# Performance work log

Hardware: AMD Instinct MI355X
Metric: run time of the kernel (lower is better)

## Reference

```python
import jax, jax.numpy as jnp
import numpy as np

HID = 256
VOCAB = 1000
REPEAT = 32
ALPHA = 1.0
LBR = 0.2
THRESH = 0.8 * ALPHA * (1.0 - LBR)  # 0.64


def _lstm_layer(x, Wih, Whh, bih, bhh):
    # x: [B,S,D]; returns hidden states [S,B,H] (torch gate order i,f,g,o)
    B = x.shape[0]
    H = Whh.shape[1]
    xg = jnp.einsum('bsd,gd->sbg', x, Wih) + (bih + bhh)  # [S,B,4H]
    def step(carry, gx):
        h, c = carry
        g = gx + h @ Whh.T
        i, f, gg, o = jnp.split(g, 4, axis=-1)
        c = jax.nn.sigmoid(f) * c + jax.nn.sigmoid(i) * jnp.tanh(gg)
        h = jax.nn.sigmoid(o) * jnp.tanh(c)
        return (h, c), h
    init = (jnp.zeros((B, H), x.dtype), jnp.zeros((B, H), x.dtype))
    _, hs = jax.lax.scan(step, init, xg)
    return hs


def _encode(x, Wih0, Whh0, bih0, bhh0, Wih1, Whh1, bih1, bhh1):
    # 2-layer LSTM (dropout inactive at inference), then sum over time -> [B,H]
    hs = _lstm_layer(x, Wih0, Whh0, bih0, bhh0)                      # [S,B,H]
    hs = _lstm_layer(jnp.transpose(hs, (1, 0, 2)), Wih1, Whh1, bih1, bhh1)
    return hs.sum(0)


def setup_inputs():
    key = jax.random.key(0)
    ks = jax.random.split(key, 20)
    B, S, D, H, P = 64, 128, 64, HID, 1024
    s = jnp.float32(0.05)
    return {
        'x1': jax.random.normal(ks[0], (B, S, D), jnp.float32),
        'x2': jax.random.normal(ks[1], (B, S, D), jnp.float32),
        'Wih0': s * jax.random.normal(ks[2], (4 * H, D), jnp.float32),
        'Whh0': s * jax.random.normal(ks[3], (4 * H, H), jnp.float32),
        'bih0': s * jax.random.normal(ks[4], (4 * H,), jnp.float32),
        'bhh0': s * jax.random.normal(ks[5], (4 * H,), jnp.float32),
        'Wih1': s * jax.random.normal(ks[6], (4 * H, H), jnp.float32),
        'Whh1': s * jax.random.normal(ks[7], (4 * H, H), jnp.float32),
        'bih1': s * jax.random.normal(ks[8], (4 * H,), jnp.float32),
        'bhh1': s * jax.random.normal(ks[9], (4 * H,), jnp.float32),
        'fc1_w': s * jax.random.normal(ks[10], (P, 2 * H), jnp.float32),
        'fc1_b': s * jax.random.normal(ks[11], (P,), jnp.float32),
        'fc2_w': s * jax.random.normal(ks[12], (P, P), jnp.float32),
        'fc2_b': s * jax.random.normal(ks[13], (P,), jnp.float32),
        'fc3_w': s * jax.random.normal(ks[14], (VOCAB * REPEAT, P), jnp.float32),
        'fc3_b': s * jax.random.normal(ks[15], (VOCAB * REPEAT,), jnp.float32),
        'bn_g': jnp.ones((P,), jnp.float32),
        'bn_b': jnp.zeros((P,), jnp.float32),
    }


def reference(x1, x2, Wih0, Whh0, bih0, bhh0, Wih1, Whh1, bih1, bhh1,
              fc1_w, fc1_b, fc2_w, fc2_b, fc3_w, fc3_b, bn_g, bn_b):
    out1 = _encode(x1, Wih0, Whh0, bih0, bhh0, Wih1, Whh1, bih1, bhh1)
    out2 = _encode(x2, Wih0, Whh0, bih0, bhh0, Wih1, Whh1, bih1, bhh1)
    h = jnp.concatenate([out1, out2], axis=1)                # [B,2H]
    h = jax.nn.gelu(h @ fc1_w.T + fc1_b, approximate=False)  # exact gelu (torch)
    h = h + jax.nn.relu(h @ fc2_w.T + fc2_b)
    # BatchNorm1d with batch statistics (training-mode normalization)
    mu = h.mean(0)
    var = h.var(0)
    h = (h - mu) / jnp.sqrt(var + 1e-5) * bn_g + bn_b
    scores = jax.nn.relu(h @ fc3_w.T + fc3_b)
    scores = scores.reshape(-1, VOCAB, REPEAT)               # [B,V,R]
    # vectorized replacement of the per-row .item() selection loop:
    # number of atoms selected per row at threshold 0.8*alpha*(1-lbr)
    num_select = jnp.maximum(1, (scores > THRESH).sum(axis=(1, 2)))
    return scores, num_select
```

## Files before the change

### kernel.cpp

```cpp
#include <hip/hip_runtime.h>
#include <cmath>


typedef _Float16 f16;
typedef _Float16 f16x8 __attribute__((ext_vector_type(8)));
typedef _Float16 f16x4 __attribute__((ext_vector_type(4)));
typedef float f32x4 __attribute__((ext_vector_type(4)));

#define MFMA(a,b,c) __builtin_amdgcn_mfma_f32_16x16x32_f16((a),(b),(c),0,0,0)
#define LSTR 280

__device__ __forceinline__ float frcp(float x) { return __builtin_amdgcn_rcpf(x); }
__device__ __forceinline__ float sigf(float x)  { return frcp(1.f + __expf(-x)); }
__device__ __forceinline__ float tanhf_(float x){ return 1.f - 2.f*frcp(__expf(2.f*x) + 1.f); }

__global__ void k_convert(const float* __restrict__ x1, const float* __restrict__ x2,
                          const float* __restrict__ Wih0, const float* __restrict__ Whh0,
                          const float* __restrict__ bih0, const float* __restrict__ bhh0,
                          const float* __restrict__ Wih1, const float* __restrict__ Whh1,
                          const float* __restrict__ bih1, const float* __restrict__ bhh1,
                          f16* __restrict__ x16, f16* __restrict__ w16, float* __restrict__ bsum,
                          int* __restrict__ flg)
{
    int i = blockIdx.x * 256 + threadIdx.x;
    if (i < 524288) { x16[i] = (f16)x1[i]; x16[524288 + i] = (f16)x2[i]; }
    if (i < 65536)  w16[i] = (f16)Wih0[i];
    if (i < 262144) {
        w16[65536  + i] = (f16)Whh0[i];
        w16[327680 + i] = (f16)Wih1[i];
        w16[589824 + i] = (f16)Whh1[i];
    }
    if (i < 1024) { bsum[i] = bih0[i] + bhh0[i]; bsum[1024 + i] = bih1[i] + bhh1[i]; }
    if (i < 64) flg[i] = 0;
}

template<int K>
__global__ __launch_bounds__(512)
void k_proj(const f16* __restrict__ A, const f16* __restrict__ Bw,
            const float* __restrict__ bias, f16* __restrict__ out)
{
    const int w = threadIdx.x >> 6, lane = threadIdx.x & 63;
    const int quad = lane >> 4, l16 = lane & 15;
    const long m0 = (long)blockIdx.x * 128 + w * 16;
    f32x4 acc[2][4] = {};
    #pragma unroll
    for (int kc = 0; kc < K/32; ++kc) {
        const int ko = kc*32 + quad*8;
        f16x8 a = *(const f16x8*)(A + (m0 + l16)*K + ko);
        #pragma unroll
        for (int tg = 0; tg < 2; ++tg) {
            const int ti = blockIdx.y*2 + tg;
            #pragma unroll
            for (int g = 0; g < 4; ++g) {
                f16x8 b = *(const f16x8*)(Bw + (long)(g*256 + ti*16 + l16)*K + ko);
                acc[tg][g] = MFMA(a, b, acc[tg][g]);
            }
        }
    }
    #pragma unroll
    for (int tg = 0; tg < 2; ++tg) {
        const int ti = blockIdx.y*2 + tg;
        float bi[4];
        #pragma unroll
        for (int g = 0; g < 4; ++g) bi[g] = bias[g*256 + ti*16 + l16];
        #pragma unroll
        for (int r = 0; r < 4; ++r) {
            long mm = m0 + quad*4 + r;
            f16x4 pv;
            #pragma unroll
            for (int g = 0; g < 4; ++g) pv[g] = (f16)(acc[tg][g][r] + bi[g]);
            *(f16x4*)(out + mm*1024 + ti*64 + l16*4) = pv;
        }
    }
}

__global__ __launch_bounds__(512, 2)
void k_mega(const f16* __restrict__ w16, const f16* __restrict__ xg0,
            f16* __restrict__ xg1, f16* __restrict__ h0s,
            const float* __restrict__ bsum1, float* __restrict__ out_enc,
            int* __restrict__ flags)
{
    __shared__ f16 wl[256*LSTR];
    __shared__ f16 hb[2*16*LSTR];
    const int tid = threadIdx.x;
    const int w = tid >> 6, lane = tid & 63;
    const int quad = lane >> 4, l16 = lane & 15;
    const int role = blockIdx.x >> 3, g = blockIdx.x & 7;

    const f16* W = (role == 0) ? w16 + 65536
                 : (role == 1) ? w16 + 327680
                               : w16 + 589824;

    f16x8 bres[6][8];
    #pragma unroll
    for (int s6 = 0; s6 < 6; ++s6) {
        const int tile = (s6 >> 1)*16 + 2*w + (s6 & 1);
        #pragma unroll
        for (int kc = 0; kc < 8; ++kc)
            bres[s6][kc] = *(const f16x8*)(W + (tile*16 + l16)*256 + kc*32 + quad*8);
    }
    {
        const int r = tid >> 1, hh = tid & 1;
        const f16* src = W + (768 + r)*256 + hh*128;
        f16* dst = wl + r*LSTR + hh*128;
        #pragma unroll
        for (int j = 0; j < 16; ++j)
            *(f16x8*)(dst + j*8) = *(const f16x8*)(src + j*8);
    }

    if (role == 1) {
        float bi[2][4];
        #pragma unroll
        for (int q = 0; q < 2; ++q)
            #pragma unroll
            for (int g4 = 0; g4 < 4; ++g4) bi[q][g4] = bsum1[g4*256 + (2*w+q)*16 + l16];
        __syncthreads();
        #pragma unroll 1
        for (int s = 0; s < 128; ++s) {
            if (tid == 0) {
                while (__hip_atomic_load(&flags[g], __ATOMIC_ACQUIRE,
                                         __HIP_MEMORY_SCOPE_AGENT) < s + 1)
                    __builtin_amdgcn_s_sleep(2);
            }
            __syncthreads();
            const f16* hrow = h0s + ((long)s*128 + g*16 + l16)*256 + quad*8;
            f16x8 av[8];
            #pragma unroll
            for (int kc = 0; kc < 8; ++kc) av[kc] = *(const f16x8*)(hrow + kc*32);
            #pragma unroll
            for (int q = 0; q < 2; ++q) {
                const int ti = 2*w + q;
                f32x4 ai = {}, af = {}, ag = {}, ao = {};
                #pragma unroll
                for (int kc = 0; kc < 8; ++kc) {
                    f16x8 bo = *(const f16x8*)(wl + (ti*16 + l16)*LSTR + kc*32 + quad*8);
                    ai = MFMA(av[kc], bres[q][kc],   ai);
                    af = MFMA(av[kc], bres[2+q][kc], af);
                    ag = MFMA(av[kc], bres[4+q][kc], ag);
                    ao = MFMA(av[kc], bo,            ao);
                }
                #pragma unroll
                for (int r = 0; r < 4; ++r) {
                    f16x4 pv;
                    pv[0] = (f16)(ai[r] + bi[q][0]);
                    pv[1] = (f16)(af[r] + bi[q][1]);
                    pv[2] = (f16)(ag[r] + bi[q][2]);
                    pv[3] = (f16)(ao[r] + bi[q][3]);
                    *(f16x4*)(xg1 + ((long)(g*16 + quad*4 + r)*128 + s)*1024
                                  + ti*64 + l16*4) = pv;
                }
            }
            __syncthreads();
            if (tid == 0)
                __hip_atomic_store(&flags[8+g], s + 1, __ATOMIC_RELEASE,
                                   __HIP_MEMORY_SCOPE_AGENT);
        }
        return;
    }

    for (int i = tid; i < 2*16*LSTR; i += 512) hb[i] = (f16)0.f;

    const f16* xg = (role == 0) ? xg0 : xg1;
    const f16* xp[4];
    #pragma unroll
    for (int r = 0; r < 4; ++r)
        xp[r] = xg + (long)(g*16 + quad*4 + r)*131072 + (2*w)*64 + l16*4;

    float c[8]    = {0,0,0,0,0,0,0,0};
    float oacc[8] = {0,0,0,0,0,0,0,0};
    __syncthreads();

    #pragma unroll 1
    for (int s = 0; s < 128; ++s) {
        const int rb = s & 1, wb = rb ^ 1;
        if (role == 2) {
            if (tid == 0) {
                while (__hip_atomic_load(&flags[8+g], __ATOMIC_ACQUIRE,
                                         __HIP_MEMORY_SCOPE_AGENT) < s + 1)
                    __builtin_amdgcn_s_sleep(2);
            }
            __syncthreads();
        }
        if (role == 0 && s > 0) {
            const int cc = tid >> 5, kk = (tid & 31) * 8;
            f16x8 hv = *(const f16x8*)(hb + (rb*16 + cc)*LSTR + kk);
            *(f16x8*)(h0s + ((long)(s-1)*128 + g*16 + cc)*256 + kk) = hv;
        }
        f16x4 xv[2][4];
        #pragma unroll
        for (int r = 0; r < 4; ++r) {
            xv[0][r] = *(const f16x4*)(xp[r]);
            xv[1][r] = *(const f16x4*)(xp[r] + 64);
        }
        #pragma unroll
        for (int q = 0; q < 2; ++q) {
            const int ti = 2*w + q;
            f32x4 ai = {}, af = {}, ag = {}, ao = {};
            #pragma unroll
            for (int kc = 0; kc < 8; ++kc) {
                f16x8 a  = *(const f16x8*)(hb + (rb*16 + l16)*LSTR + kc*32 + quad*8);
                f16x8 bo = *(const f16x8*)(wl + (ti*16 + l16)*LSTR + kc*32 + quad*8);
                ai = MFMA(a, bres[q][kc],   ai);
                af = MFMA(a, bres[2+q][kc], af);
                ag = MFMA(a, bres[4+q][kc], ag);
                ao = MFMA(a, bo,            ao);
            }
            #pragma unroll
            for (int r = 0; r < 4; ++r) {
                float gi = sigf(ai[r] + (float)xv[q][r][0]);
                float gf = sigf(af[r] + (float)xv[q][r][1]);
                float gg = tanhf_(ag[r] + (float)xv[q][r][2]);
                float go = sigf(ao[r] + (float)xv[q][r][3]);
                const int ci = q*4 + r;
                float cn = gf*c[ci] + gi*gg;
                c[ci] = cn;
                float hn = go * tanhf_(cn);
                if (role == 2) oacc[ci] += hn;
                hb[(wb*16 + quad*4 + r)*LSTR + ti*16 + l16] = (f16)hn;
            }
        }
        #pragma unroll
        for (int r = 0; r < 4; ++r) xp[r] += 1024;
        __syncthreads();
        if (role == 0 && tid == 0)
            __hip_atomic_store(&flags[g], s, __ATOMIC_RELEASE,
                               __HIP_MEMORY_SCOPE_AGENT);
    }
    if (role == 0) {
        const int cc = tid >> 5, kk = (tid & 31) * 8;
        f16x8 hv = *(const f16x8*)(hb + (0*16 + cc)*LSTR + kk);
        *(f16x8*)(h0s + ((long)127*128 + g*16 + cc)*256 + kk) = hv;
        __syncthreads();
        if (tid == 0)
            __hip_atomic_store(&flags[g], 128, __ATOMIC_RELEASE,
                               __HIP_MEMORY_SCOPE_AGENT);
    }
    if (role == 2) {
        #pragma unroll
        for (int q = 0; q < 2; ++q)
            #pragma unroll
            for (int r = 0; r < 4; ++r)
                out_enc[(long)(g*16 + quad*4 + r)*256 + (2*w+q)*16 + l16] = oacc[q*4 + r];
    }
}

template<int K, int MODE>
__global__ __launch_bounds__(256)
void k_fc(const float* __restrict__ A, const float* __restrict__ W,
          const float* __restrict__ bias, const float* __restrict__ res,
          float* __restrict__ out, const int Nst)
{
    __shared__ float ws[32*64];
    __shared__ float as[64*64];
    const int tid = threadIdx.x;
    const int n0 = blockIdx.x * 32;
    const int m2 = tid & 31, ndg = tid >> 5;
    float acc[2][4] = {};
    for (int kc = 0; kc < K/64; ++kc) {
        __syncthreads();
        {
            const int col = tid >> 3, k8 = (tid & 7)*8;
            const float* src = W + (long)(n0 + col)*K + kc*64 + k8;
            *(float4*)(ws + col*64 + k8)     = *(const float4*)(src);
            *(float4*)(ws + col*64 + k8 + 4) = *(const float4*)(src + 4);
        }
        {
            const int m = tid >> 2, j4 = (tid & 3)*16;
            #pragma unroll
            for (int i4 = 0; i4 < 4; ++i4) {
                const int kk = kc*64 + j4 + i4*4;
                const float* srcA;
                if (MODE == 0) srcA = (kk < 256) ? (A + (long)m*256 + kk)
                                                 : (A + 16384 + (long)m*256 + kk - 256);
                else           srcA = A + (long)m*K + kk;
                float4 v = *(const float4*)srcA;
                as[(j4 + i4*4 + 0)*64 + m] = v.x;
                as[(j4 + i4*4 + 1)*64 + m] = v.y;
                as[(j4 + i4*4 + 2)*64 + m] = v.z;
                as[(j4 + i4*4 + 3)*64 + m] = v.w;
            }
        }
        __syncthreads();
        #pragma unroll 4
        for (int k4 = 0; k4 < 64; k4 += 4) {
            float a0[4], a1[4];
            #pragma unroll
            for (int i = 0; i < 4; ++i) {
                a0[i] = as[(k4+i)*64 + m2];
                a1[i] = as[(k4+i)*64 + m2 + 32];
            }
            #pragma unroll
            for (int j = 0; j < 4; ++j) {
                const float4 wv = *(const float4*)(ws + (ndg*4 + j)*64 + k4);
                acc[0][j] += a0[0]*wv.x + a0[1]*wv.y + a0[2]*wv.z + a0[3]*wv.w;
                acc[1][j] += a1[0]*wv.x + a1[1]*wv.y + a1[2]*wv.z + a1[3]*wv.w;
            }
        }
    }
    #pragma unroll
    for (int i = 0; i < 2; ++i) {
        const int m = m2 + i*32;
        #pragma unroll
        for (int j = 0; j < 4; ++j) {
            const int nn = n0 + ndg*4 + j;
            float v = acc[i][j] + bias[nn];
            if (MODE == 0)      v = 0.5f * v * (1.0f + erff(v * 0.7071067811865475f));
            else if (MODE == 1) v = res[(long)m*1024 + nn] + fmaxf(v, 0.f);
            else                v = fmaxf(v, 0.f);
            out[(long)m*Nst + nn] = v;
        }
    }
}

__global__ void k_bn(const float* __restrict__ h2, const float* __restrict__ g,
                     const float* __restrict__ b, float* __restrict__ h3)
{
    const int col = blockIdx.x*256 + threadIdx.x;
    float s = 0.f, ss = 0.f;
    for (int m = 0; m < 64; ++m) { float v = h2[m*1024 + col]; s += v; ss += v*v; }
    const float mu  = s * (1.f/64.f);
    const float var = ss * (1.f/64.f) - mu*mu;
    const float rs  = rsqrtf(var + 1e-5f);
    const float gg = g[col], bb = b[col];
    for (int m = 0; m < 64; ++m) {
        float v = h2[m*1024 + col];
        h3[m*1024 + col] = (v - mu)*rs*gg + bb;
    }
}

__global__ void k_count(const float* __restrict__ scores, float* __restrict__ outc)
{
    const int row = blockIdx.x, tid = threadIdx.x;
    const float* p = scores + (long)row*32000;
    int cnt = 0;
    for (int i = tid; i < 32000; i += 256)
        cnt += ((double)p[i] > 0.6400000000000001) ? 1 : 0;
    __shared__ int red[256];
    red[tid] = cnt; __syncthreads();
    for (int off = 128; off > 0; off >>= 1) {
        if (tid < off) red[tid] += red[tid + off];
        __syncthreads();
    }
    if (tid == 0) outc[row] = (float)(red[0] < 1 ? 1 : red[0]);
}

extern "C" void kernel_launch(void* const* d_in, const int* in_sizes, int n_in,
                              void* d_out, int out_size, void* d_ws, size_t ws_size,
                              hipStream_t stream)
{
    const float* x1    = (const float*)d_in[0];
    const float* x2    = (const float*)d_in[1];
    const float* Wih0  = (const float*)d_in[2];
    const float* Whh0  = (const float*)d_in[3];
    const float* bih0  = (const float*)d_in[4];
    const float* bhh0  = (const float*)d_in[5];
    const float* Wih1  = (const float*)d_in[6];
    const float* Whh1  = (const float*)d_in[7];
    const float* bih1  = (const float*)d_in[8];
    const float* bhh1  = (const float*)d_in[9];
    const float* fc1_w = (const float*)d_in[10];
    const float* fc1_b = (const float*)d_in[11];
    const float* fc2_w = (const float*)d_in[12];
    const float* fc2_b = (const float*)d_in[13];
    const float* fc3_w = (const float*)d_in[14];
    const float* fc3_b = (const float*)d_in[15];
    const float* bn_g  = (const float*)d_in[16];
    const float* bn_b  = (const float*)d_in[17];
    float* out = (float*)d_out;

    char* ws = (char*)d_ws;
    f16*   x16   = (f16*)(ws);
    f16*   w16   = (f16*)(ws + 2097152);
    float* bsum  = (float*)(ws + 3801088);
    int*   flags = (int*)(ws + 3809280);
    float* enc   = (float*)(ws + 3809536);
    f16*   h0s   = (f16*)(ws + 3940608);
    f16*   xg0   = (f16*)(ws + 12329216);
    f16*   xg1   = (f16*)(ws + 45883648);
    float* h1    = (float*)(ws + 12329216);
    float* h2    = (float*)(ws + 12591360);
    float* h3    = (float*)(ws + 12853504);

    k_convert<<<2048, 256, 0, stream>>>(x1,x2,Wih0,Whh0,bih0,bhh0,Wih1,Whh1,bih1,bhh1,
                                        x16, w16, bsum, flags);
    k_proj<64><<<dim3(128,8), 512, 0, stream>>>(x16, w16, bsum, xg0);
    k_mega<<<24, 512, 0, stream>>>(w16, xg0, xg1, h0s, bsum + 1024, enc, flags);
    k_fc<512,0><<<32, 256, 0, stream>>>(enc, fc1_w, fc1_b, nullptr, h1, 1024);
    k_fc<1024,1><<<32, 256, 0, stream>>>(h1, fc2_w, fc2_b, h1, h2, 1024);
    k_bn<<<4, 256, 0, stream>>>(h2, bn_g, bn_b, h3);
    k_fc<1024,2><<<1000, 256, 0, stream>>>(h3, fc3_w, fc3_b, nullptr, out, 32000);
    k_count<<<64, 256, 0, stream>>>(out, out + 2048000);
}
```

Before: 1.036 ms.

## Batch LSTM cross-block flag handshakes every two steps and fuse BatchNorm into fc2

The producer/consumer flag synchronisation between the layer-0 recurrence, the layer-1 input projection and the layer-1 recurrence blocks now happens every two timesteps instead of every step. Spin-waits use relaxed polling followed by a single acquire load. Separately, the BatchNorm statistics and normalisation are fused into the fc2 epilogue through a shared-memory transpose, which removes the k_bn launch and one intermediate buffer. This lowers per-step synchronisation latency in the serial critical path, at the cost of coarser pipelining granularity between stages.

```diff
diff --git a/kernel.cpp b/kernel.cpp
--- a/kernel.cpp
+++ b/kernel.cpp
@@ -13,6 +13,12 @@
 __device__ __forceinline__ float frcp(float x) { return __builtin_amdgcn_rcpf(x); }
 __device__ __forceinline__ float sigf(float x)  { return frcp(1.f + __expf(-x)); }
 __device__ __forceinline__ float tanhf_(float x){ return 1.f - 2.f*frcp(__expf(2.f*x) + 1.f); }
+
+__device__ __forceinline__ void wait_flag(int* f, int target) {
+    while (__hip_atomic_load(f, __ATOMIC_RELAXED, __HIP_MEMORY_SCOPE_AGENT) < target)
+        __builtin_amdgcn_s_sleep(1);
+    (void)__hip_atomic_load(f, __ATOMIC_ACQUIRE, __HIP_MEMORY_SCOPE_AGENT);
+}
 
 __global__ void k_convert(const float* __restrict__ x1, const float* __restrict__ x2,
                           const float* __restrict__ Wih0, const float* __restrict__ Whh0,
@@ -117,12 +123,10 @@
         __syncthreads();
         #pragma unroll 1
         for (int s = 0; s < 128; ++s) {
-            if (tid == 0) {
-                while (__hip_atomic_load(&flags[g], __ATOMIC_ACQUIRE,
-                                         __HIP_MEMORY_SCOPE_AGENT) < s + 1)
-                    __builtin_amdgcn_s_sleep(2);
-            }
-            __syncthreads();
+            if ((s & 1) == 0) {
+                if (tid == 0) wait_flag(&flags[g], s + 2);
+                __syncthreads();
+            }
             const f16* hrow = h0s + ((long)s*128 + g*16 + l16)*256 + quad*8;
             f16x8 av[8];
             #pragma unroll
@@ -150,10 +154,12 @@
                                   + ti*64 + l16*4) = pv;
                 }
             }
-            __syncthreads();
-            if (tid == 0)
-                __hip_atomic_store(&flags[8+g], s + 1, __ATOMIC_RELEASE,
-                                   __HIP_MEMORY_SCOPE_AGENT);
+            if (s & 1) {
+                __syncthreads();
+                if (tid == 0)
+                    __hip_atomic_store(&flags[8+g], s + 1, __ATOMIC_RELEASE,
+                                       __HIP_MEMORY_SCOPE_AGENT);
+            }
         }
         return;
     }
@@ -173,12 +179,8 @@
     #pragma unroll 1
     for (int s = 0; s < 128; ++s) {
         const int rb = s & 1, wb = rb ^ 1;
-        if (role == 2) {
-            if (tid == 0) {
-                while (__hip_atomic_load(&flags[8+g], __ATOMIC_ACQUIRE,
-                                         __HIP_MEMORY_SCOPE_AGENT) < s + 1)
-                    __builtin_amdgcn_s_sleep(2);
-            }
+        if (role == 2 && (s & 1) == 0) {
+            if (tid == 0) wait_flag(&flags[8+g], s + 2);
             __syncthreads();
         }
         if (role == 0 && s > 0) {
@@ -222,7 +224,7 @@
         #pragma unroll
         for (int r = 0; r < 4; ++r) xp[r] += 1024;
         __syncthreads();
-        if (role == 0 && tid == 0)
+        if (role == 0 && (s & 1) == 0 && s > 0 && tid == 0)
             __hip_atomic_store(&flags[g], s, __ATOMIC_RELEASE,
                                __HIP_MEMORY_SCOPE_AGENT);
     }
@@ -248,10 +250,12 @@
 __global__ __launch_bounds__(256)
 void k_fc(const float* __restrict__ A, const float* __restrict__ W,
           const float* __restrict__ bias, const float* __restrict__ res,
+          const float* __restrict__ bng, const float* __restrict__ bnb,
           float* __restrict__ out, const int Nst)
 {
     __shared__ float ws[32*64];
     __shared__ float as[64*64];
+    __shared__ float mus[32], rss[32];
     const int tid = threadIdx.x;
     const int n0 = blockIdx.x * 32;
     const int m2 = tid & 31, ndg = tid >> 5;
@@ -297,6 +301,43 @@
             }
         }
     }
+    if (MODE == 1) {
+        float vv[2][4];
+        #pragma unroll
+        for (int i = 0; i < 2; ++i)
+            #pragma unroll
+            for (int j = 0; j < 4; ++j) {
+                const int m = m2 + i*32, nn = n0 + ndg*4 + j;
+                vv[i][j] = res[(long)m*1024 + nn] + fmaxf(acc[i][j] + bias[nn], 0.f);
+            }
+        __syncthreads();
+        #pragma unroll
+        for (int i = 0; i < 2; ++i)
+            #pragma unroll
+            for (int j = 0; j < 4; ++j)
+                as[(m2 + i*32)*33 + ndg*4 + j] = vv[i][j];
+        __syncthreads();
+        if (tid < 32) {
+            float s = 0.f, ss = 0.f;
+            #pragma unroll 4
+            for (int m = 0; m < 64; ++m) {
+                float x = as[m*33 + tid];
+                s += x; ss += x*x;
+            }
+            const float mu = s * (1.f/64.f);
+            mus[tid] = mu;
+            rss[tid] = rsqrtf(ss * (1.f/64.f) - mu*mu + 1e-5f);
+        }
+        __syncthreads();
+        #pragma unroll
+        for (int i = 0; i < 2; ++i)
+            #pragma unroll
+            for (int j = 0; j < 4; ++j) {
+                const int m = m2 + i*32, cl = ndg*4 + j, nn = n0 + cl;
+                out[(long)m*Nst + nn] = (vv[i][j] - mus[cl]) * rss[cl] * bng[nn] + bnb[nn];
+            }
+        return;
+    }
     #pragma unroll
     for (int i = 0; i < 2; ++i) {
         const int m = m2 + i*32;
@@ -304,27 +345,10 @@
         for (int j = 0; j < 4; ++j) {
             const int nn = n0 + ndg*4 + j;
             float v = acc[i][j] + bias[nn];
-            if (MODE == 0)      v = 0.5f * v * (1.0f + erff(v * 0.7071067811865475f));
-            else if (MODE == 1) v = res[(long)m*1024 + nn] + fmaxf(v, 0.f);
-            else                v = fmaxf(v, 0.f);
+            if (MODE == 0) v = 0.5f * v * (1.0f + erff(v * 0.7071067811865475f));
+            else           v = fmaxf(v, 0.f);
             out[(long)m*Nst + nn] = v;
         }
-    }
-}
-
-__global__ void k_bn(const float* __restrict__ h2, const float* __restrict__ g,
-                     const float* __restrict__ b, float* __restrict__ h3)
-{
-    const int col = blockIdx.x*256 + threadIdx.x;
-    float s = 0.f, ss = 0.f;
-    for (int m = 0; m < 64; ++m) { float v = h2[m*1024 + col]; s += v; ss += v*v; }
-    const float mu  = s * (1.f/64.f);
-    const float var = ss * (1.f/64.f) - mu*mu;
-    const float rs  = rsqrtf(var + 1e-5f);
-    const float gg = g[col], bb = b[col];
-    for (int m = 0; m < 64; ++m) {
-        float v = h2[m*1024 + col];
-        h3[m*1024 + col] = (v - mu)*rs*gg + bb;
     }
 }
 
@@ -378,16 +402,14 @@
     f16*   xg0   = (f16*)(ws + 12329216);
     f16*   xg1   = (f16*)(ws + 45883648);
     float* h1    = (float*)(ws + 12329216);
-    float* h2    = (float*)(ws + 12591360);
-    float* h3    = (float*)(ws + 12853504);
+    float* h3    = (float*)(ws + 12591360);
 
     k_convert<<<2048, 256, 0, stream>>>(x1,x2,Wih0,Whh0,bih0,bhh0,Wih1,Whh1,bih1,bhh1,
                                         x16, w16, bsum, flags);
     k_proj<64><<<dim3(128,8), 512, 0, stream>>>(x16, w16, bsum, xg0);
     k_mega<<<24, 512, 0, stream>>>(w16, xg0, xg1, h0s, bsum + 1024, enc, flags);
-    k_fc<512,0><<<32, 256, 0, stream>>>(enc, fc1_w, fc1_b, nullptr, h1, 1024);
-    k_fc<1024,1><<<32, 256, 0, stream>>>(h1, fc2_w, fc2_b, h1, h2, 1024);
-    k_bn<<<4, 256, 0, stream>>>(h2, bn_g, bn_b, h3);
-    k_fc<1024,2><<<1000, 256, 0, stream>>>(h3, fc3_w, fc3_b, nullptr, out, 32000);
+    k_fc<512,0><<<32, 256, 0, stream>>>(enc, fc1_w, fc1_b, nullptr, nullptr, nullptr, h1, 1024);
+    k_fc<1024,1><<<32, 256, 0, stream>>>(h1, fc2_w, fc2_b, h1, bn_g, bn_b, h3, 1024);
+    k_fc<1024,2><<<1000, 256, 0, stream>>>(h3, fc3_w, fc3_b, nullptr, nullptr, nullptr, out, 32000);
     k_count<<<64, 256, 0, stream>>>(out, out + 2048000);
 }
```

After: 987.4 us. -4.7%, faster.
